# Performance work log

Hardware: AMD Instinct MI355X
Metric: run time of the kernel (lower is better)

The kernel has to match this reference:

```python
import jax, jax.numpy as jnp
import numpy as np

K = 3          # deformable conv kernel size
DG = 4         # deformable groups
PAD = (K - 1) // 2


def _deform_conv(x, offset, w, dg=DG, pad=PAD):
    """DCNv1 forward (stride=1, dilation=1, conv groups=1, no bias).

    x:      [B, C, H, W]
    offset: [B, dg*K*K*2, H, W]  layout per group: (dy, dx) per kernel tap
    w:      [O, C, K, K]
    """
    B, C, H, W = x.shape
    O = w.shape[0]
    k2 = K * K
    gC = C // dg

    off = offset.reshape(B, dg, k2, 2, H, W)
    dy, dx = off[:, :, :, 0], off[:, :, :, 1]          # [B, dg, k2, H, W]

    ky, kx = jnp.meshgrid(jnp.arange(K), jnp.arange(K), indexing='ij')
    ky = ky.reshape(k2).astype(x.dtype)
    kx = kx.reshape(k2).astype(x.dtype)
    hi = jnp.arange(H, dtype=x.dtype)
    wi = jnp.arange(W, dtype=x.dtype)

    # absolute fractional sample coords: p0 - pad + kernel tap + learned offset
    ys = hi[None, None, None, :, None] - pad + ky[None, None, :, None, None] + dy
    xs = wi[None, None, None, None, :] - pad + kx[None, None, :, None, None] + dx

    y0 = jnp.floor(ys)
    x0 = jnp.floor(xs)
    ly = ys - y0   # bilinear weights
    lx = xs - x0
    y0 = y0.astype(jnp.int32)
    x0 = x0.astype(jnp.int32)

    xg = x.reshape(B, dg, gC, H * W)

    def gather(yi, xi):
        # zero padding outside the image (per-corner validity, matches mmcv)
        valid = ((yi >= 0) & (yi < H) & (xi >= 0) & (xi < W)).astype(x.dtype)
        idx = (jnp.clip(yi, 0, H - 1) * W + jnp.clip(xi, 0, W - 1)).reshape(B, dg, -1)
        vals = jax.vmap(jax.vmap(lambda t, i: t[:, i]))(xg, idx)  # [B,dg,gC,k2*H*W]
        return vals.reshape(B, dg, gC, k2, H, W) * valid[:, :, None]

    # bilinear interpolation of the 4 corners
    sampled = ((1 - ly) * (1 - lx))[:, :, None] * gather(y0,     x0) \
            + ((1 - ly) * lx      )[:, :, None] * gather(y0,     x0 + 1) \
            + (ly       * (1 - lx))[:, :, None] * gather(y0 + 1, x0) \
            + (ly       * lx      )[:, :, None] * gather(y0 + 1, x0 + 1)
    # sampled: [B, dg, gC, k2, H, W]

    wr = w.reshape(O, dg, gC, k2)
    return jnp.einsum('bgckhw,ogck->bohw', sampled, wr)


def setup_inputs() -> dict:
    key = jax.random.key(0)
    k0, k1, k2k, k3 = jax.random.split(key, 4)
    B, C, H, W, O = 2, 256, 128, 128, 256
    oc = DG * K * K * 2
    x = jax.random.normal(k0, (B, C, H, W), jnp.float32)
    # offset conv is zero-init in the module; use small random values so the
    # deformable sampling path is actually exercised
    w_offset = jax.random.normal(k1, (oc, C, 1, 1), jnp.float32) * 0.01
    b_offset = jax.random.normal(k2k, (oc,), jnp.float32) * 0.01
    w_deform = jax.random.normal(k3, (O, C, K, K), jnp.float32) / np.sqrt(C * K * K)
    return {"x": x, "w_offset": w_offset, "b_offset": b_offset, "w_deform": w_deform}


def reference(x, w_offset, b_offset, w_deform):
    # 1x1 conv predicting offsets
    offset = jnp.einsum('bchw,oc->bohw', x, w_offset[:, :, 0, 0]) \
             + b_offset[None, :, None, None]
    # deformable conv + ReLU
    return jax.nn.relu(_deform_conv(x, offset, w_deform))
```

## Files before the change

kernel.cpp:

```cpp
#include <hip/hip_runtime.h>

#define HW 16384

typedef _Float16 f16;
typedef __attribute__((ext_vector_type(4))) float f32x4;
typedef __attribute__((ext_vector_type(8))) _Float16 f16x8;
typedef __attribute__((ext_vector_type(4))) int i32x4;

union h8i4 { f16x8 h; i32x4 i; };

static __device__ __forceinline__ int pk_f16(float lo, float hi) {
    int r;
    asm("v_cvt_pkrtz_f16_f32 %0, %1, %2" : "=v"(r) : "v"(lo), "v"(hi));
    return r;
}
static __device__ __forceinline__ f16 ush2h(unsigned short u) {
    union { unsigned short s; f16 h; } c; c.s = u; return c.h;
}

__global__ __launch_bounds__(256) void prep_kernel(
    const float* __restrict__ x, const float* __restrict__ wd,
    const float* __restrict__ woff,
    f16* __restrict__ xT, f16* __restrict__ Wc2, f16* __restrict__ Wo2)
{
    int bid = blockIdx.x;
    int tid = threadIdx.x;
    if (bid < 2048) {
        __shared__ float tl[64][65];
        int ct = bid & 3, pt = (bid >> 2) & 255, b = bid >> 10;
        const float* xb = x + ((size_t)(b * 256 + ct * 64)) * HW + pt * 64;
        #pragma unroll
        for (int j = 0; j < 4; ++j) {
            int slot = tid + j * 256;
            int c = slot >> 4, p4 = slot & 15;
            float4 v = *(const float4*)(xb + (size_t)c * HW + p4 * 4);
            tl[c][p4 * 4 + 0] = v.x;
            tl[c][p4 * 4 + 1] = v.y;
            tl[c][p4 * 4 + 2] = v.z;
            tl[c][p4 * 4 + 3] = v.w;
        }
        __syncthreads();
        f16* ob = xT + ((size_t)(b * HW + pt * 64)) * 256 + ct * 64;
        #pragma unroll
        for (int j2 = 0; j2 < 2; ++j2) {
            int slot = tid + j2 * 256;
            int p = slot >> 3, sl = slot & 7;
            i32x4 st;
            #pragma unroll
            for (int kq = 0; kq < 4; ++kq)
                ((int*)&st)[kq] = pk_f16(tl[sl*8 + kq*2][p], tl[sl*8 + kq*2 + 1][p]);
            *(i32x4*)(ob + (size_t)p * 256 + sl * 8) = st;
        }
    } else if (bid < 2336) {
        int slot = (bid - 2048) * 256 + tid;
        int l  = slot & 63;
        int ks = (slot >> 6) & 1;
        int mi = (slot >> 7) & 3;
        int q4 = (slot >> 9) & 3;
        int kc = slot >> 11;
        int g = kc / 9, tap = kc - g * 9;
        int o = q4 * 64 + mi * 16 + (l & 15);
        int cgb = (ks * 4 + (l >> 4)) * 8;
        f16* dst = Wc2 + (size_t)slot * 8;
        const float* src = wd + (size_t)o * 2304 + tap;
        #pragma unroll
        for (int e = 0; e < 8; ++e)
            dst[e] = (f16)(src[(size_t)(g * 64 + cgb + e) * 9]);
    } else {
        int slot = (bid - 2336) * 256 + tid;
        int kk = slot / 320;
        int rem = slot - kk * 320;
        int o = rem >> 2, jq = rem & 3;
        f16* dst = Wo2 + (size_t)slot * 8;
        #pragma unroll
        for (int e = 0; e < 8; ++e)
            dst[e] = (o < 72) ? (f16)(woff[(size_t)o * 256 + kk * 32 + jq * 8 + e]) : (f16)0.f;
    }
}

__global__ __launch_bounds__(512, 4) void deform_kernel(
    const f16* __restrict__ xT, const f16* __restrict__ Wc2,
    const f16* __restrict__ Wo2, const float* __restrict__ b_off,
    float* __restrict__ out)
{
    __shared__ __align__(16) i32x4 pk[2304];
    __shared__ __align__(16) short Sbuf[2][4096];

    const int t    = threadIdx.x;
    const int lane = t & 63;
    const int q    = t >> 6;
    const int lr   = lane & 15, lq = lane >> 4;
    int bid = blockIdx.x;
    bid = (bid & 7) * 64 + (bid >> 3);
    const int gp0  = bid << 6;
    const int b    = gp0 >> 14;
    const int hw0  = gp0 & 16383;
    const int h    = hw0 >> 7;
    const int w0   = hw0 & 127;

    {
        const int p16 = (q & 3) * 16;
        f16x8 xv[8];
        const f16* xrow = xT + ((size_t)(b * HW + hw0 + p16 + lr)) * 256 + lq * 8;
        #pragma unroll
        for (int kk = 0; kk < 8; ++kk)
            xv[kk] = *(const f16x8*)(xrow + kk * 32);
        const int mi0 = (q < 4) ? 0 : 3;
        const int nmi = (q < 4) ? 3 : 2;
        for (int im = 0; im < nmi; ++im) {
            int mi = mi0 + im;
            f32x4 oa = (f32x4)0.f;
            #pragma unroll
            for (int kk = 0; kk < 8; ++kk) {
                f16x8 af = *(const f16x8*)(Wo2 + (size_t)((kk * 80 + mi * 16 + lr) * 32 + lq * 8));
                oa = __builtin_amdgcn_mfma_f32_16x16x32_f16(af, xv[kk], oa, 0, 0, 0);
            }
            #pragma unroll
            for (int ri = 0; ri < 2; ++ri) {
                int gt = mi * 8 + lq * 2 + ri;
                if (gt < 36) {
                    int p = p16 + lr;
                    float dy = oa[ri * 2]     + b_off[2 * gt];
                    float dx = oa[ri * 2 + 1] + b_off[2 * gt + 1];
                    int tap = gt % 9;
                    float ys = (float)(h - 1 + tap / 3) + dy;
                    float xs = (float)(w0 + p - 1 + tap % 3) + dx;
                    float fy = floorf(ys), fx = floorf(xs);
                    int y0 = (int)fy, x0 = (int)fx;
                    float ly = ys - fy, lx = xs - fx;
                    float omy = 1.f - ly, omx = 1.f - lx;
                    float vy0 = ((unsigned)y0       < 128u) ? 1.f : 0.f;
                    float vy1 = ((unsigned)(y0 + 1) < 128u) ? 1.f : 0.f;
                    float vx0 = ((unsigned)x0       < 128u) ? 1.f : 0.f;
                    float vx1 = ((unsigned)(x0 + 1) < 128u) ? 1.f : 0.f;
                    int y0c = min(max(y0, 0), 127), y1c = min(max(y0 + 1, 0), 127);
                    int x0c = min(max(x0, 0), 127), x1c = min(max(x0 + 1, 0), 127);
                    i32x4 e;
                    e.x = y0c * 128 + x0c;
                    e.y = y1c * 128 + x1c;
                    e.z = pk_f16(omy * omx * vy0 * vx0, omy * lx * vy0 * vx1);
                    e.w = pk_f16(ly  * omx * vy1 * vx0, ly  * lx * vy1 * vx1);
                    pk[gt * 64 + p] = e;
                }
            }
        }
    }
    __syncthreads();

    f32x4 acc[2][4];
    #pragma unroll
    for (int mi = 0; mi < 2; ++mi)
        #pragma unroll
        for (int nj = 0; nj < 4; ++nj)
            acc[mi][nj] = (f32x4)0.f;

    const f16* xbase = xT + ((size_t)b * HW) * 256;
    const int ppix = q * 8 + (lane >> 3);
    const int sl   = lane & 7;
    const int q4   = q >> 1;
    const int mo   = (q & 1) * 2;

    {
        i32x4 cd = pk[ppix];
        int idx00 = cd.x, idx11 = cd.y;
        int idx01 = (idx00 & ~127) | (idx11 & 127);
        int idx10 = (idx11 & ~127) | (idx00 & 127);
        f16x8 w00v = (f16x8)ush2h((unsigned short)(cd.z & 0xffff));
        f16x8 w01v = (f16x8)ush2h((unsigned short)((unsigned)cd.z >> 16));
        f16x8 w10v = (f16x8)ush2h((unsigned short)(cd.w & 0xffff));
        f16x8 w11v = (f16x8)ush2h((unsigned short)((unsigned)cd.w >> 16));
        const f16* cb = xbase + sl * 8;
        f16x8 sv = *(const f16x8*)(cb + (size_t)idx00 * 256) * w00v;
        sv += *(const f16x8*)(cb + (size_t)idx01 * 256) * w01v;
        sv += *(const f16x8*)(cb + (size_t)idx10 * 256) * w10v;
        sv += *(const f16x8*)(cb + (size_t)idx11 * 256) * w11v;
        h8i4 u; u.h = sv;
        ((i32x4*)Sbuf[0])[ppix * 8 + (sl ^ (ppix & 7))] = u.i;
    }
    __syncthreads();

    short* Sc = Sbuf[0];
    short* Sn = Sbuf[1];

    for (int kc = 0; kc < 36; ++kc) {
        f16x8 v00, v01, v10, v11;
        f16x8 w00v, w01v, w10v, w11v;
        const bool pf = (kc < 35);
        if (pf) {
            int kn = kc + 1;
            int g  = kn / 9;
            i32x4 cd = pk[kn * 64 + ppix];
            int idx00 = cd.x, idx11 = cd.y;
            int idx01 = (idx00 & ~127) | (idx11 & 127);
            int idx10 = (idx11 & ~127) | (idx00 & 127);
            w00v = (f16x8)ush2h((unsigned short)(cd.z & 0xffff));
            w01v = (f16x8)ush2h((unsigned short)((unsigned)cd.z >> 16));
            w10v = (f16x8)ush2h((unsigned short)(cd.w & 0xffff));
            w11v = (f16x8)ush2h((unsigned short)((unsigned)cd.w >> 16));
            const f16* cb = xbase + (size_t)(g * 64 + sl * 8);
            v00 = *(const f16x8*)(cb + (size_t)idx00 * 256);
            v01 = *(const f16x8*)(cb + (size_t)idx01 * 256);
            v10 = *(const f16x8*)(cb + (size_t)idx10 * 256);
            v11 = *(const f16x8*)(cb + (size_t)idx11 * 256);
        }
        {
            f16x8 a_[2][2];
            const f16* wb = Wc2 + ((size_t)kc * 2048 + q4 * 512 + mo * 128 + lane) * 8;
            #pragma unroll
            for (int mi = 0; mi < 2; ++mi)
                #pragma unroll
                for (int ks = 0; ks < 2; ++ks)
                    a_[mi][ks] = *(const f16x8*)(wb + (mi * 128 + ks * 64) * 8);
            #pragma unroll
            for (int ks = 0; ks < 2; ++ks) {
                f16x8 bb[4];
                #pragma unroll
                for (int nj = 0; nj < 4; ++nj) {
                    int pp = nj * 16 + lr;
                    h8i4 u;
                    u.i = ((const i32x4*)Sc)[pp * 8 + ((ks * 4 + lq) ^ (pp & 7))];
                    bb[nj] = u.h;
                }
                #pragma unroll
                for (int mi = 0; mi < 2; ++mi)
                    #pragma unroll
                    for (int nj = 0; nj < 4; ++nj)
                        acc[mi][nj] = __builtin_amdgcn_mfma_f32_16x16x32_f16(
                            a_[mi][ks], bb[nj], acc[mi][nj], 0, 0, 0);
            }
        }
        if (pf) {
            f16x8 sv = v00 * w00v;
            sv += v01 * w01v;
            sv += v10 * w10v;
            sv += v11 * w11v;
            h8i4 u; u.h = sv;
            ((i32x4*)Sn)[ppix * 8 + (sl ^ (ppix & 7))] = u.i;
        }
        __syncthreads();
        short* tmp = Sc; Sc = Sn; Sn = tmp;
    }

    #pragma unroll
    for (int mi = 0; mi < 2; ++mi)
        #pragma unroll
        for (int nj = 0; nj < 4; ++nj)
            #pragma unroll
            for (int r = 0; r < 4; ++r) {
                int o  = q * 32 + mi * 16 + lq * 4 + r;
                int pp = nj * 16 + lr;
                out[((size_t)(b * 256 + o) << 14) + hw0 + pp] = fmaxf(acc[mi][nj][r], 0.f);
            }
}

extern "C" void kernel_launch(void* const* d_in, const int* in_sizes, int n_in,
                              void* d_out, int out_size, void* d_ws, size_t ws_size,
                              hipStream_t stream) {
    const float* x     = (const float*)d_in[0];
    const float* w_off = (const float*)d_in[1];
    const float* b_off = (const float*)d_in[2];
    const float* w_def = (const float*)d_in[3];
    float* out = (float*)d_out;

    f16* xT  = (f16*)d_ws;
    f16* Wc2 = (f16*)((char*)d_ws + 16777216);
    f16* Wo2 = (f16*)((char*)d_ws + 17956864);

    prep_kernel<<<2346, 256, 0, stream>>>(x, w_def, w_off, xT, Wc2, Wo2);
    deform_kernel<<<512, 512, 0, stream>>>(xT, Wc2, Wo2, b_off, out);
}
```

Measured before the change: 148.5 us.

## Pipeline two gather chunks per barrier with deeper prefetch and MFMA priority

```diff
diff --git a/kernel.cpp b/kernel.cpp
--- a/kernel.cpp
+++ b/kernel.cpp
@@ -78,13 +78,15 @@
     }
 }
 
+struct GS { f16x8 v00, v01, v10, v11; int wz, ww; };
+
 __global__ __launch_bounds__(512, 4) void deform_kernel(
     const f16* __restrict__ xT, const f16* __restrict__ Wc2,
     const f16* __restrict__ Wo2, const float* __restrict__ b_off,
     float* __restrict__ out)
 {
-    __shared__ __align__(16) i32x4 pk[2304];
-    __shared__ __align__(16) short Sbuf[2][4096];
+    __shared__ __align__(16) i32x4 pkt[2304];
+    __shared__ __align__(16) short Sbuf[2][8192];
 
     const int t    = threadIdx.x;
     const int lane = t & 63;
@@ -140,7 +142,7 @@
                     e.y = y1c * 128 + x1c;
                     e.z = pk_f16(omy * omx * vy0 * vx0, omy * lx * vy0 * vx1);
                     e.w = pk_f16(ly  * omx * vy1 * vx0, ly  * lx * vy1 * vx1);
-                    pk[gt * 64 + p] = e;
+                    pkt[gt * 64 + p] = e;
                 }
             }
         }
@@ -160,85 +162,77 @@
     const int q4   = q >> 1;
     const int mo   = (q & 1) * 2;
 
-    {
-        i32x4 cd = pk[ppix];
+    auto issue_chunk = [&](int kc, GS& gs) {
+        int grp = kc / 9;
+        i32x4 cd = pkt[kc * 64 + ppix];
         int idx00 = cd.x, idx11 = cd.y;
         int idx01 = (idx00 & ~127) | (idx11 & 127);
         int idx10 = (idx11 & ~127) | (idx00 & 127);
-        f16x8 w00v = (f16x8)ush2h((unsigned short)(cd.z & 0xffff));
-        f16x8 w01v = (f16x8)ush2h((unsigned short)((unsigned)cd.z >> 16));
-        f16x8 w10v = (f16x8)ush2h((unsigned short)(cd.w & 0xffff));
-        f16x8 w11v = (f16x8)ush2h((unsigned short)((unsigned)cd.w >> 16));
-        const f16* cb = xbase + sl * 8;
-        f16x8 sv = *(const f16x8*)(cb + (size_t)idx00 * 256) * w00v;
-        sv += *(const f16x8*)(cb + (size_t)idx01 * 256) * w01v;
-        sv += *(const f16x8*)(cb + (size_t)idx10 * 256) * w10v;
-        sv += *(const f16x8*)(cb + (size_t)idx11 * 256) * w11v;
+        const f16* cb = xbase + (size_t)(grp * 64 + sl * 8);
+        gs.v00 = *(const f16x8*)(cb + (size_t)idx00 * 256);
+        gs.v01 = *(const f16x8*)(cb + (size_t)idx01 * 256);
+        gs.v10 = *(const f16x8*)(cb + (size_t)idx10 * 256);
+        gs.v11 = *(const f16x8*)(cb + (size_t)idx11 * 256);
+        gs.wz = cd.z; gs.ww = cd.w;
+    };
+    auto interp_chunk = [&](const GS& gs, short* Sh) {
+        f16x8 w00v = (f16x8)ush2h((unsigned short)(gs.wz & 0xffff));
+        f16x8 w01v = (f16x8)ush2h((unsigned short)((unsigned)gs.wz >> 16));
+        f16x8 w10v = (f16x8)ush2h((unsigned short)(gs.ww & 0xffff));
+        f16x8 w11v = (f16x8)ush2h((unsigned short)((unsigned)gs.ww >> 16));
+        f16x8 sv = gs.v00 * w00v;
+        sv += gs.v01 * w01v;
+        sv += gs.v10 * w10v;
+        sv += gs.v11 * w11v;
         h8i4 u; u.h = sv;
-        ((i32x4*)Sbuf[0])[ppix * 8 + (sl ^ (ppix & 7))] = u.i;
-    }
-    __syncthreads();
-
-    short* Sc = Sbuf[0];
-    short* Sn = Sbuf[1];
-
-    for (int kc = 0; kc < 36; ++kc) {
-        f16x8 v00, v01, v10, v11;
-        f16x8 w00v, w01v, w10v, w11v;
-        const bool pf = (kc < 35);
-        if (pf) {
-            int kn = kc + 1;
-            int g  = kn / 9;
-            i32x4 cd = pk[kn * 64 + ppix];
-            int idx00 = cd.x, idx11 = cd.y;
-            int idx01 = (idx00 & ~127) | (idx11 & 127);
-            int idx10 = (idx11 & ~127) | (idx00 & 127);
-            w00v = (f16x8)ush2h((unsigned short)(cd.z & 0xffff));
-            w01v = (f16x8)ush2h((unsigned short)((unsigned)cd.z >> 16));
-            w10v = (f16x8)ush2h((unsigned short)(cd.w & 0xffff));
-            w11v = (f16x8)ush2h((unsigned short)((unsigned)cd.w >> 16));
-            const f16* cb = xbase + (size_t)(g * 64 + sl * 8);
-            v00 = *(const f16x8*)(cb + (size_t)idx00 * 256);
-            v01 = *(const f16x8*)(cb + (size_t)idx01 * 256);
-            v10 = *(const f16x8*)(cb + (size_t)idx10 * 256);
-            v11 = *(const f16x8*)(cb + (size_t)idx11 * 256);
-        }
-        {
-            f16x8 a_[2][2];
-            const f16* wb = Wc2 + ((size_t)kc * 2048 + q4 * 512 + mo * 128 + lane) * 8;
+        ((i32x4*)Sh)[ppix * 8 + (sl ^ (ppix & 7))] = u.i;
+    };
+    auto mfma_chunk = [&](int kc, const short* Sh) {
+        f16x8 a_[2][2];
+        const f16* wb = Wc2 + ((size_t)kc * 2048 + q4 * 512 + mo * 128 + lane) * 8;
+        #pragma unroll
+        for (int mi = 0; mi < 2; ++mi)
+            #pragma unroll
+            for (int ks = 0; ks < 2; ++ks)
+                a_[mi][ks] = *(const f16x8*)(wb + (mi * 128 + ks * 64) * 8);
+        #pragma unroll
+        for (int ks = 0; ks < 2; ++ks) {
+            f16x8 bb[4];
+            #pragma unroll
+            for (int nj = 0; nj < 4; ++nj) {
+                int pp = nj * 16 + lr;
+                h8i4 u;
+                u.i = ((const i32x4*)Sh)[pp * 8 + ((ks * 4 + lq) ^ (pp & 7))];
+                bb[nj] = u.h;
+            }
             #pragma unroll
             for (int mi = 0; mi < 2; ++mi)
                 #pragma unroll
-                for (int ks = 0; ks < 2; ++ks)
-                    a_[mi][ks] = *(const f16x8*)(wb + (mi * 128 + ks * 64) * 8);
-            #pragma unroll
-            for (int ks = 0; ks < 2; ++ks) {
-                f16x8 bb[4];
-                #pragma unroll
-                for (int nj = 0; nj < 4; ++nj) {
-                    int pp = nj * 16 + lr;
-                    h8i4 u;
-                    u.i = ((const i32x4*)Sc)[pp * 8 + ((ks * 4 + lq) ^ (pp & 7))];
-                    bb[nj] = u.h;
-                }
-                #pragma unroll
-                for (int mi = 0; mi < 2; ++mi)
-                    #pragma unroll
-                    for (int nj = 0; nj < 4; ++nj)
-                        acc[mi][nj] = __builtin_amdgcn_mfma_f32_16x16x32_f16(
-                            a_[mi][ks], bb[nj], acc[mi][nj], 0, 0, 0);
-            }
-        }
-        if (pf) {
-            f16x8 sv = v00 * w00v;
-            sv += v01 * w01v;
-            sv += v10 * w10v;
-            sv += v11 * w11v;
-            h8i4 u; u.h = sv;
-            ((i32x4*)Sn)[ppix * 8 + (sl ^ (ppix & 7))] = u.i;
-        }
+                for (int nj = 0; nj < 4; ++nj)
+                    acc[mi][nj] = __builtin_amdgcn_mfma_f32_16x16x32_f16(
+                        a_[mi][ks], bb[nj], acc[mi][nj], 0, 0, 0);
+        }
+    };
+
+    GS A0, A1, B0, B1;
+    issue_chunk(0, A0); issue_chunk(1, A1);
+
+    for (int s = 0; s < 18; s += 2) {
+        const int c0 = s * 2;
+        issue_chunk(c0 + 2, B0); issue_chunk(c0 + 3, B1);
+        interp_chunk(A0, Sbuf[0]); interp_chunk(A1, Sbuf[0] + 4096);
         __syncthreads();
-        short* tmp = Sc; Sc = Sn; Sn = tmp;
+        __builtin_amdgcn_s_setprio(1);
+        mfma_chunk(c0,     Sbuf[0]);
+        mfma_chunk(c0 + 1, Sbuf[0] + 4096);
+        __builtin_amdgcn_s_setprio(0);
+        if (s < 16) { issue_chunk(c0 + 4, A0); issue_chunk(c0 + 5, A1); }
+        interp_chunk(B0, Sbuf[1]); interp_chunk(B1, Sbuf[1] + 4096);
+        __syncthreads();
+        __builtin_amdgcn_s_setprio(1);
+        mfma_chunk(c0 + 2, Sbuf[1]);
+        mfma_chunk(c0 + 3, Sbuf[1] + 4096);
+        __builtin_amdgcn_s_setprio(0);
     }
 
     #pragma unroll
```

Result: slower. 203.5 us (+37.0%).
